# Kernel tuning notes

Hardware: AMD Instinct MI355X
Metric: run time of the kernel (lower is better)

Reference implementation:

```python
import jax, jax.numpy as jnp
import numpy as np

HEADS = 8
DIM_HEAD = 64
SCALE = DIM_HEAD ** (-0.5)


def setup_inputs() -> dict:
    key = jax.random.key(0)
    k1, k2, k3 = jax.random.split(key, 3)
    b, l, c = 8, 4096, 512
    x = jax.random.normal(k1, (b, l, c), dtype=jnp.float32)
    w_qkv = jax.random.normal(k2, (3 * c, c), dtype=jnp.float32) * (c ** -0.5)
    w_out = jax.random.normal(k3, (c, c), dtype=jnp.float32) * (c ** -0.5)
    b_out = jnp.zeros((c,), dtype=jnp.float32)
    return {"x": x, "w_qkv": w_qkv, "w_out": w_out, "b_out": b_out}


def reference(x, w_qkv, w_out, b_out):
    b, l, c = x.shape
    h = HEADS
    lh = l // h
    # to_qkv: Linear(dim, 3*dim, bias=False)
    qkv = x @ w_qkv.T                                   # (b, l, 3c)
    qkv = qkv.reshape(b, lh, h, 3, c).transpose(3, 0, 2, 1, 4)  # (3, b, h, l/h, c)
    q, k, v = qkv[0], qkv[1], qkv[2]                    # each (b, h, l/h, c)
    # transpose(-2,-1): attention is over the CHANNEL axis
    q = jnp.swapaxes(q, -2, -1)                         # (b, h, c, l/h)
    k = jnp.swapaxes(k, -2, -1)                         # (b, h, c, l/h)
    v = jnp.swapaxes(v, -2, -1)                         # (b, h, c, l/h)
    attn = jnp.einsum('bhcl,bhdl->bhcd', q, k) * SCALE  # (b, h, c, c)
    attn = jax.nn.softmax(attn, axis=-1)
    y = jnp.einsum('bhcd,bhdl->bhcl', attn, v)          # (b, h, c, l/h)
    y = y.transpose(0, 3, 1, 2).reshape(b, l, c)        # (b, l/h, h, c) -> (b, l, c)
    # to_out: Linear(dim, dim) + Dropout (identity at eval)
    out = y @ w_out.T + b_out
    return out
```

## Files before the change

kernel.cpp:

```cpp
#include <hip/hip_runtime.h>
#include <stdint.h>
#include <stddef.h>

typedef _Float16 f16;
typedef _Float16 f16x8 __attribute__((ext_vector_type(8)));
typedef _Float16 f16x4 __attribute__((ext_vector_type(4)));
typedef float f32x4 __attribute__((ext_vector_type(4)));

__device__ __forceinline__ void gload16(const void* g, void* l) {
    auto gp = (const __attribute__((address_space(1))) uint32_t*)(uintptr_t)g;
    auto lp = (__attribute__((address_space(3))) uint32_t*)(uintptr_t)l;
    __builtin_amdgcn_global_load_lds(gp, lp, 16, 0, 0);
}

__device__ __forceinline__ f16x4 cvt4(f32x4 v) {
    return f16x4{ (f16)v[0], (f16)v[1], (f16)v[2], (f16)v[3] };
}

__global__ __launch_bounds__(256) void prep_k(const float* __restrict__ x,
                                              const float* __restrict__ wqkv,
                                              const float* __restrict__ wout,
                                              f16* __restrict__ xb,
                                              f16* __restrict__ wqb,
                                              f16* __restrict__ wob) {
    int tid = blockIdx.x * blockDim.x + threadIdx.x;
    int stride = gridDim.x * blockDim.x;
    for (int i = tid; i < 4194304; i += stride) {
        float4 v = ((const float4*)x)[i];
        *(f16x4*)(xb + (size_t)i * 4) = f16x4{ (f16)v.x, (f16)v.y, (f16)v.z, (f16)v.w };
    }
    for (int i = tid; i < 196608; i += stride) {
        float4 v = ((const float4*)wqkv)[i];
        *(f16x4*)(wqb + (size_t)i * 4) = f16x4{ (f16)v.x, (f16)v.y, (f16)v.z, (f16)v.w };
    }
    for (int i = tid; i < 65536; i += stride) {
        float4 v = ((const float4*)wout)[i];
        *(f16x4*)(wob + (size_t)i * 4) = f16x4{ (f16)v.x, (f16)v.y, (f16)v.z, (f16)v.w };
    }
}


#define STAGE(SB) do {                                                          \
    gload16(Ab + kb + soff,          &ldsA[SB][( 0 + wid*8)*64]);               \
    gload16(Ab + kb + soff + 65536,  &ldsA[SB][( 64 + wid*8)*64]);              \
    gload16(Ab + kb + soff + 131072, &ldsA[SB][(128 + wid*8)*64]);              \
    gload16(Ab + kb + soff + 196608, &ldsA[SB][(192 + wid*8)*64]);              \
    gload16(Bb + kb + soff,          &ldsB[SB][( 0 + wid*8)*64]);               \
    gload16(Bb + kb + soff + 65536,  &ldsB[SB][( 64 + wid*8)*64]);              \
    kb += 128;                                                                  \
} while (0)

#define RD(SET, BUF) do {                                                       \
    _Pragma("unroll") for (int mi = 0; mi < 4; ++mi)                            \
    _Pragma("unroll") for (int kk = 0; kk < 2; ++kk)                            \
        aF##SET[mi][kk] = *(const f16x8*)(&ldsA[BUF][0] + aoff[mi][kk]);        \
    _Pragma("unroll") for (int ni = 0; ni < 4; ++ni)                            \
    _Pragma("unroll") for (int kk = 0; kk < 2; ++kk)                            \
        bF##SET[ni][kk] = *(const f16x8*)(&ldsB[BUF][0] + boff[ni][kk]);        \
} while (0)

#define MM(SET, KK, ML, MH_) do {                                               \
    __builtin_amdgcn_s_setprio(1);                                              \
    _Pragma("unroll") for (int mi = ML; mi < MH_; ++mi)                         \
    _Pragma("unroll") for (int ni = 0; ni < 4; ++ni) {                          \
        if constexpr (SWP)                                                      \
            acc[mi][ni] = __builtin_amdgcn_mfma_f32_16x16x32_f16(               \
                bF##SET[ni][KK], aF##SET[mi][KK], acc[mi][ni], 0, 0, 0);        \
        else                                                                    \
            acc[mi][ni] = __builtin_amdgcn_mfma_f32_16x16x32_f16(               \
                aF##SET[mi][KK], bF##SET[ni][KK], acc[mi][ni], 0, 0, 0);        \
    }                                                                           \
    __builtin_amdgcn_s_setprio(0);                                              \
} while (0)

#define MM3(SET)   do { MM(SET, 0, 0, 2); MM(SET, 0, 2, 4); MM(SET, 1, 0, 2); } while (0)
#define MMLAST(SET) MM(SET, 1, 2, 4)
#define W6  asm volatile("s_waitcnt vmcnt(6)" ::: "memory")
#define W0  asm volatile("s_waitcnt vmcnt(0)" ::: "memory")
#define BAR __builtin_amdgcn_s_barrier()

template <int MODE, bool SWP, bool QK>
__global__ __launch_bounds__(512) void g9_k(const f16* __restrict__ A0,
                                            const f16* __restrict__ B0,
                                            void* __restrict__ C0,
                                            void* __restrict__ C1,
                                            const float* __restrict__ bias) {
    __shared__ f16 ldsA[3][16384];
    __shared__ f16 ldsB[3][8192];

    const int tid = threadIdx.x;
    const int lane = tid & 63;
    const int wid = tid >> 6;
    const int wr = wid >> 1;
    const int wc = wid & 1;

    const int bid = blockIdx.x;
    int tm, tn, bh = 0;
    if constexpr (MODE == 0 && QK) {
        int swz = (bid & 7) * 128 + (bid >> 3);
        tm = (swz >> 3) * 256; tn = (swz & 7) * 128;
    } else if constexpr (MODE == 0) {
        int swz = (bid & 7) * 64 + (bid >> 3);
        tm = (swz >> 2) * 256; tn = (swz & 3) * 128;
    } else if constexpr (MODE == 1 || MODE == 2) {
        int swz = (bid & 7) * 64 + (bid >> 3);
        bh = swz >> 3; tm = ((swz >> 2) & 1) * 256; tn = (swz & 3) * 128;
    } else {
        int swz = (bid & 7) * 64 + (bid >> 3);
        tm = (swz >> 2) * 256; tn = (swz & 3) * 128;
    }

    const size_t bhoff = (MODE == 1 || MODE == 2) ? (size_t)bh * 262144 : 0;
    const char* Ab = (const char*)(A0 + bhoff + (size_t)tm * 512);
    const char* Bb = (const char*)(B0 + bhoff + (size_t)tn * 512);

    const int c8s = (tid & 7) ^ (((tid >> 3) & 7) ^ wid);
    const int soff = (tid >> 3) * 1024 + c8s * 16;
    int kb = 0;

    int aoff[4][2], boff[4][2];
#pragma unroll
    for (int mi = 0; mi < 4; ++mi) {
        int r;
        if constexpr (QK) {
            int e = wr * 4 + mi;
            r = (lane & 15) * 8 + (e >> 3) * 128 + (e & 7);
        } else {
            r = wr * 64 + mi * 16 + (lane & 15);
        }
#pragma unroll
        for (int kk = 0; kk < 2; ++kk) {
            int c8 = (lane >> 4) + kk * 4;
            aoff[mi][kk] = r * 64 + (c8 ^ ((r & 7) ^ ((r >> 3) & 7))) * 8;
        }
    }
#pragma unroll
    for (int ni = 0; ni < 4; ++ni) {
        int r = wc * 64 + ni * 16 + (lane & 15);
#pragma unroll
        for (int kk = 0; kk < 2; ++kk) {
            int c8 = (lane >> 4) + kk * 4;
            boff[ni][kk] = r * 64 + (c8 ^ ((r & 7) ^ ((r >> 3) & 7))) * 8;
        }
    }

    f32x4 acc[4][4] = {};
    f16x8 aF0[4][2], bF0[4][2], aF1[4][2], bF1[4][2];

    STAGE(0); STAGE(1);
    W6; BAR;
    RD(0, 0);

    STAGE(2); MM3(0); W6; BAR; RD(1, 1); MMLAST(0);
    STAGE(0); MM3(1); W6; BAR; RD(0, 2); MMLAST(1);
    STAGE(1); MM3(0); W6; BAR; RD(1, 0); MMLAST(0);
    STAGE(2); MM3(1); W6; BAR; RD(0, 1); MMLAST(1);
    STAGE(0); MM3(0); W6; BAR; RD(1, 2); MMLAST(0);
    STAGE(1); MM3(1); W6; BAR; RD(0, 0); MMLAST(1);
              MM3(0); W0; BAR; RD(1, 1); MMLAST(0);
              MM3(1);                    MMLAST(1);

    if constexpr (MODE == 0 && QK) {
        const int b = tm >> 12;
        const int lt = (tm & 4095) >> 3;
        f16* dst = (f16*)(tn < 512 ? C0 : C1);
        const int cb = (tn & 511) + wc * 64;
#pragma unroll
        for (int mi = 0; mi < 4; ++mi) {
            int e = wr * 4 + mi;
            int h = e & 7;
            int lh0 = lt + (e >> 3) * 16 + (lane >> 4) * 4;
#pragma unroll
            for (int ni = 0; ni < 4; ++ni) {
                int c = cb + ni * 16 + (lane & 15);
                *(f16x4*)(dst + ((size_t)((b * 8 + h) * 512 + c)) * 512 + lh0) =
                    cvt4(acc[mi][ni]);
            }
        }
    } else if constexpr (MODE == 0) {
        f16* dst = (f16*)C0;
#pragma unroll
        for (int mi = 0; mi < 4; ++mi) {
            int t = tm + wr * 64 + mi * 16 + (lane & 15);
            int b = t >> 12, l = t & 4095;
            int h = l & 7, lh = l >> 3;
#pragma unroll
            for (int ni = 0; ni < 4; ++ni) {
                int d0 = tn + wc * 64 + ni * 16 + (lane >> 4) * 4;
                *(f16x4*)(dst + ((size_t)((b * 8 + h) * 512 + lh)) * 512 + d0) =
                    cvt4(acc[mi][ni]);
            }
        }
    } else if constexpr (MODE == 1) {
        f16* S = (f16*)C0 + (size_t)bh * 262144;
#pragma unroll
        for (int mi = 0; mi < 4; ++mi) {
            int cm = tm + wr * 64 + mi * 16 + (lane & 15);
#pragma unroll
            for (int ni = 0; ni < 4; ++ni) {
                int d0 = tn + wc * 64 + ni * 16 + (lane >> 4) * 4;
                *(f16x4*)(S + (size_t)cm * 512 + d0) = cvt4(acc[mi][ni] * 0.125f);
            }
        }
    } else if constexpr (MODE == 2) {
        f16* yb = (f16*)C0;
        const int b = bh >> 3, h = bh & 7;
#pragma unroll
        for (int mi = 0; mi < 4; ++mi) {
            int c0 = tm + wr * 64 + mi * 16 + (lane >> 4) * 4;
#pragma unroll
            for (int ni = 0; ni < 4; ++ni) {
                int l = tn + wc * 64 + ni * 16 + (lane & 15);
                size_t tok = (size_t)b * 4096 + (size_t)l * 8 + h;
                *(f16x4*)(yb + tok * 512 + c0) = cvt4(acc[mi][ni]);
            }
        }
    } else {
        float* O = (float*)C0;
#pragma unroll
        for (int mi = 0; mi < 4; ++mi) {
            int m = tm + wr * 64 + mi * 16 + (lane & 15);
#pragma unroll
            for (int ni = 0; ni < 4; ++ni) {
                int n0 = tn + wc * 64 + ni * 16 + (lane >> 4) * 4;
                float4 bv = *(const float4*)(bias + n0);
                f32x4 v = acc[mi][ni];
                v[0] += bv.x; v[1] += bv.y; v[2] += bv.z; v[3] += bv.w;
                *(f32x4*)(O + (size_t)m * 512 + n0) = v;
            }
        }
    }
}

__global__ __launch_bounds__(256) void softmax_k(const f16* __restrict__ S,
                                                 f16* __restrict__ P) {
    int row = blockIdx.x * 4 + (threadIdx.x >> 6);
    int lane = threadIdx.x & 63;
    f16x8 v = *(const f16x8*)(S + (size_t)row * 512 + lane * 8);
    float f[8];
#pragma unroll
    for (int i = 0; i < 8; ++i) f[i] = (float)v[i];
    float m = f[0];
#pragma unroll
    for (int i = 1; i < 8; ++i) m = fmaxf(m, f[i]);
#pragma unroll
    for (int off = 1; off < 64; off <<= 1) m = fmaxf(m, __shfl_xor(m, off, 64));
    float s = 0.f, e[8];
#pragma unroll
    for (int i = 0; i < 8; ++i) { e[i] = __expf(f[i] - m); s += e[i]; }
#pragma unroll
    for (int off = 1; off < 64; off <<= 1) s += __shfl_xor(s, off, 64);
    float inv = 1.0f / s;
    f16x8 pk;
#pragma unroll
    for (int i = 0; i < 8; ++i) pk[i] = (f16)(e[i] * inv);
    *(f16x8*)(P + (size_t)row * 512 + lane * 8) = pk;
}

extern "C" void kernel_launch(void* const* d_in, const int* in_sizes, int n_in,
                              void* d_out, int out_size, void* d_ws, size_t ws_size,
                              hipStream_t stream) {
    const float* x = (const float*)d_in[0];
    const float* wqkv = (const float*)d_in[1];
    const float* wout = (const float*)d_in[2];
    const float* bout = (const float*)d_in[3];
    float* out = (float*)d_out;
    char* ws = (char*)d_ws;
    const size_t MBs = 1u << 20;

    f16* xb  = (f16*)(ws + 0);
    f16* wqb = (f16*)(ws + 32 * MBs);
    f16* wob = (f16*)(ws + 34 * MBs);
    f16* Qb  = (f16*)(ws + 35 * MBs);
    f16* Kb  = (f16*)(ws + 67 * MBs);
    f16* Vb  = (f16*)(ws + 99 * MBs);
    f16* Sb  = (f16*)(ws + 131 * MBs);
    f16* Pb  = xb;
    f16* yb  = Qb;

    prep_k<<<1024, 256, 0, stream>>>(x, wqkv, wout, xb, wqb, wob);
    g9_k<0, false, true><<<1024, 512, 0, stream>>>(xb, wqb, Qb, Kb, nullptr);
    g9_k<0, true, false><<<512, 512, 0, stream>>>(xb, wqb + (size_t)1024 * 512, Vb, nullptr, nullptr);
    g9_k<1, true, false><<<512, 512, 0, stream>>>(Qb, Kb, Sb, nullptr, nullptr);
    softmax_k<<<8192, 256, 0, stream>>>(Sb, Pb);
    g9_k<2, false, false><<<512, 512, 0, stream>>>(Pb, Vb, yb, nullptr, nullptr);
    g9_k<3, true, false><<<512, 512, 0, stream>>>(yb, wob, out, nullptr, bout);
}
```

Before: 201.3 us.

## Shrink GEMM tiles to 128x128 with 256-thread blocks and double buffering

Replaces the 256x128-tile, 512-thread, triple-buffered GEMM kernel with a 128x128-tile, 256-thread kernel that double-buffers LDS and targets two blocks per CU. Grid sizes double for every GEMM launch, and the staging swizzle and QK row mapping are adjusted to the smaller tile. The aim is more resident blocks and better load balance across CUs, but each tile gets less operand reuse and the loop now waits with vmcnt(0) at every step, which gives up some load/compute overlap.

```diff
diff --git a/kernel.cpp b/kernel.cpp
--- a/kernel.cpp
+++ b/kernel.cpp
@@ -40,13 +40,15 @@
 }
 
 
-#define STAGE(SB) do {                                                          \
-    gload16(Ab + kb + soff,          &ldsA[SB][( 0 + wid*8)*64]);               \
-    gload16(Ab + kb + soff + 65536,  &ldsA[SB][( 64 + wid*8)*64]);              \
-    gload16(Ab + kb + soff + 131072, &ldsA[SB][(128 + wid*8)*64]);              \
-    gload16(Ab + kb + soff + 196608, &ldsA[SB][(192 + wid*8)*64]);              \
-    gload16(Bb + kb + soff,          &ldsB[SB][( 0 + wid*8)*64]);               \
-    gload16(Bb + kb + soff + 65536,  &ldsB[SB][( 64 + wid*8)*64]);              \
+#define STAGE(NB) do {                                                          \
+    gload16(Ab + kb + sE,          &ldsA[NB][( 0 + wid*8)*64]);                 \
+    gload16(Ab + kb + sO + 32768,  &ldsA[NB][(32 + wid*8)*64]);                 \
+    gload16(Ab + kb + sE + 65536,  &ldsA[NB][(64 + wid*8)*64]);                 \
+    gload16(Ab + kb + sO + 98304,  &ldsA[NB][(96 + wid*8)*64]);                 \
+    gload16(Bb + kb + sE,          &ldsB[NB][( 0 + wid*8)*64]);                 \
+    gload16(Bb + kb + sO + 32768,  &ldsB[NB][(32 + wid*8)*64]);                 \
+    gload16(Bb + kb + sE + 65536,  &ldsB[NB][(64 + wid*8)*64]);                 \
+    gload16(Bb + kb + sO + 98304,  &ldsB[NB][(96 + wid*8)*64]);                 \
     kb += 128;                                                                  \
 } while (0)
 
@@ -75,18 +77,24 @@
 
 #define MM3(SET)   do { MM(SET, 0, 0, 2); MM(SET, 0, 2, 4); MM(SET, 1, 0, 2); } while (0)
 #define MMLAST(SET) MM(SET, 1, 2, 4)
-#define W6  asm volatile("s_waitcnt vmcnt(6)" ::: "memory")
 #define W0  asm volatile("s_waitcnt vmcnt(0)" ::: "memory")
 #define BAR __builtin_amdgcn_s_barrier()
 
+#define TILE(CUR, NXT, NB, STG, FINAL) do {                                     \
+    if (STG) STAGE(NB);                                                         \
+    MM3(CUR);                                                                   \
+    if (!FINAL) { W0; BAR; RD(NXT, NB); }                                       \
+    MMLAST(CUR);                                                                \
+} while (0)
+
 template <int MODE, bool SWP, bool QK>
-__global__ __launch_bounds__(512) void g9_k(const f16* __restrict__ A0,
-                                            const f16* __restrict__ B0,
-                                            void* __restrict__ C0,
-                                            void* __restrict__ C1,
-                                            const float* __restrict__ bias) {
-    __shared__ f16 ldsA[3][16384];
-    __shared__ f16 ldsB[3][8192];
+__global__ __launch_bounds__(256, 2) void g10_k(const f16* __restrict__ A0,
+                                                const f16* __restrict__ B0,
+                                                void* __restrict__ C0,
+                                                void* __restrict__ C1,
+                                                const float* __restrict__ bias) {
+    __shared__ f16 ldsA[2][8192];
+    __shared__ f16 ldsB[2][8192];
 
     const int tid = threadIdx.x;
     const int lane = tid & 63;
@@ -97,25 +105,27 @@
     const int bid = blockIdx.x;
     int tm, tn, bh = 0;
     if constexpr (MODE == 0 && QK) {
+        int swz = (bid & 7) * 256 + (bid >> 3);
+        tm = (swz >> 3) * 128; tn = (swz & 7) * 128;
+    } else if constexpr (MODE == 0) {
         int swz = (bid & 7) * 128 + (bid >> 3);
-        tm = (swz >> 3) * 256; tn = (swz & 7) * 128;
-    } else if constexpr (MODE == 0) {
-        int swz = (bid & 7) * 64 + (bid >> 3);
-        tm = (swz >> 2) * 256; tn = (swz & 3) * 128;
+        tm = (swz >> 2) * 128; tn = (swz & 3) * 128;
     } else if constexpr (MODE == 1 || MODE == 2) {
-        int swz = (bid & 7) * 64 + (bid >> 3);
-        bh = swz >> 3; tm = ((swz >> 2) & 1) * 256; tn = (swz & 3) * 128;
+        int swz = (bid & 7) * 128 + (bid >> 3);
+        bh = swz >> 4; tm = ((swz >> 2) & 3) * 128; tn = (swz & 3) * 128;
     } else {
-        int swz = (bid & 7) * 64 + (bid >> 3);
-        tm = (swz >> 2) * 256; tn = (swz & 3) * 128;
+        int swz = (bid & 7) * 128 + (bid >> 3);
+        tm = (swz >> 2) * 128; tn = (swz & 3) * 128;
     }
 
     const size_t bhoff = (MODE == 1 || MODE == 2) ? (size_t)bh * 262144 : 0;
     const char* Ab = (const char*)(A0 + bhoff + (size_t)tm * 512);
     const char* Bb = (const char*)(B0 + bhoff + (size_t)tn * 512);
 
-    const int c8s = (tid & 7) ^ (((tid >> 3) & 7) ^ wid);
-    const int soff = (tid >> 3) * 1024 + c8s * 16;
+    const int u = tid >> 3;
+    const int colE = ((tid & 7) ^ ((u & 7) ^ (u >> 3))) * 16;
+    const int sE = u * 1024 + colE;
+    const int sO = sE ^ 64;
     int kb = 0;
 
     int aoff[4][2], boff[4][2];
@@ -123,8 +133,7 @@
     for (int mi = 0; mi < 4; ++mi) {
         int r;
         if constexpr (QK) {
-            int e = wr * 4 + mi;
-            r = (lane & 15) * 8 + (e >> 3) * 128 + (e & 7);
+            r = (lane & 15) * 8 + wr * 4 + mi;
         } else {
             r = wr * 64 + mi * 16 + (lane & 15);
         }
@@ -147,29 +156,27 @@
     f32x4 acc[4][4] = {};
     f16x8 aF0[4][2], bF0[4][2], aF1[4][2], bF1[4][2];
 
-    STAGE(0); STAGE(1);
-    W6; BAR;
+    STAGE(0);
+    W0; BAR;
     RD(0, 0);
 
-    STAGE(2); MM3(0); W6; BAR; RD(1, 1); MMLAST(0);
-    STAGE(0); MM3(1); W6; BAR; RD(0, 2); MMLAST(1);
-    STAGE(1); MM3(0); W6; BAR; RD(1, 0); MMLAST(0);
-    STAGE(2); MM3(1); W6; BAR; RD(0, 1); MMLAST(1);
-    STAGE(0); MM3(0); W6; BAR; RD(1, 2); MMLAST(0);
-    STAGE(1); MM3(1); W6; BAR; RD(0, 0); MMLAST(1);
-              MM3(0); W0; BAR; RD(1, 1); MMLAST(0);
-              MM3(1);                    MMLAST(1);
+#pragma unroll 1
+    for (int i = 0; i < 3; ++i) {
+        TILE(0, 1, 1, true, false);
+        TILE(1, 0, 0, true, false);
+    }
+    TILE(0, 1, 1, true, false);
+    TILE(1, 1, 1, false, true);
 
     if constexpr (MODE == 0 && QK) {
         const int b = tm >> 12;
         const int lt = (tm & 4095) >> 3;
         f16* dst = (f16*)(tn < 512 ? C0 : C1);
         const int cb = (tn & 511) + wc * 64;
-#pragma unroll
-        for (int mi = 0; mi < 4; ++mi) {
-            int e = wr * 4 + mi;
-            int h = e & 7;
-            int lh0 = lt + (e >> 3) * 16 + (lane >> 4) * 4;
+        const int lh0 = lt + (lane >> 4) * 4;
+#pragma unroll
+        for (int mi = 0; mi < 4; ++mi) {
+            int h = wr * 4 + mi;
 #pragma unroll
             for (int ni = 0; ni < 4; ++ni) {
                 int c = cb + ni * 16 + (lane & 15);
@@ -279,10 +286,10 @@
     f16* yb  = Qb;
 
     prep_k<<<1024, 256, 0, stream>>>(x, wqkv, wout, xb, wqb, wob);
-    g9_k<0, false, true><<<1024, 512, 0, stream>>>(xb, wqb, Qb, Kb, nullptr);
-    g9_k<0, true, false><<<512, 512, 0, stream>>>(xb, wqb + (size_t)1024 * 512, Vb, nullptr, nullptr);
-    g9_k<1, true, false><<<512, 512, 0, stream>>>(Qb, Kb, Sb, nullptr, nullptr);
+    g10_k<0, false, true><<<2048, 256, 0, stream>>>(xb, wqb, Qb, Kb, nullptr);
+    g10_k<0, true, false><<<1024, 256, 0, stream>>>(xb, wqb + (size_t)1024 * 512, Vb, nullptr, nullptr);
+    g10_k<1, true, false><<<1024, 256, 0, stream>>>(Qb, Kb, Sb, nullptr, nullptr);
     softmax_k<<<8192, 256, 0, stream>>>(Sb, Pb);
-    g9_k<2, false, false><<<512, 512, 0, stream>>>(Pb, Vb, yb, nullptr, nullptr);
-    g9_k<3, true, false><<<512, 512, 0, stream>>>(yb, wob, out, nullptr, bout);
-}
+    g10_k<2, false, false><<<1024, 256, 0, stream>>>(Pb, Vb, yb, nullptr, nullptr);
+    g10_k<3, true, false><<<1024, 256, 0, stream>>>(yb, wob, out, nullptr, bout);
+}
```

Result: no change. 198.3 us (-1.5%).
